# Kernel optimization log

Measured on AMD Instinct MI355X. Metric: run time of the kernel, lower is better.

The kernel has to match this reference:

```python
import jax, jax.numpy as jnp
import numpy as np

B = 48            # graph pairs
NQ, NC = 20, 16   # query / corpus node counts (corpus padded to NMAX)
NMAX = 20         # max_node_set_size
DN, DE = 16, 8    # raw node / edge feature dims
D = 32            # node_state_dim
EH = 64           # edge_hidden_sizes[-1]
EQ, EC = 80, 60   # edges per query / corpus graph
PROP = 5          # n_prop_layers
TEMP = 0.01       # sinkhorn temperature
ITERS = 20        # sinkhorn iterations
LAMBDA = 1.0
NTOT = B * (NQ + NC)
NE = B * (EQ + EC)
SRC, DST = np.triu_indices(NMAX, 1)   # nC2 = 190 node pairs
_indq = np.ones(NMAX, np.int32)
_indc = np.array([1] * NC + [0] * (NMAX - NC), np.int32)
NXOR = jnp.asarray((_indq[:, None] ^ _indc[None, :]).astype(np.float32))  # [20,20]


def _mlp2(x, w1, b1, w2, b2):
    return jnp.maximum(x @ w1 + b1, 0.0) @ w2 + b2


def _sinkhorn(log_alpha):
    la = log_alpha / TEMP
    for _ in range(ITERS):
        la = la - jax.nn.logsumexp(la, axis=2, keepdims=True)
        la = la - jax.nn.logsumexp(la, axis=1, keepdims=True)
    return jnp.exp(la)


def _edge_emb(H, adj, w1, b1, w2, b2):
    s, d = H[:, SRC], H[:, DST]            # [B,nC2,D] gathers
    e = adj[:, SRC, DST][..., None]        # [B,nC2,1]
    f = _mlp2(jnp.concatenate([s, d, e], -1), w1, b1, w2, b2)
    bk = _mlp2(jnp.concatenate([d, s, e], -1), w1, b1, w2, b2)
    return f + bk                          # bidirectional msg, [B,nC2,EH]


def _forward(node_features, edge_features, query_adj, corpus_adj,
             enc_nw, enc_nb, enc_ew, enc_eb,
             msg_w1, msg_b1, msg_w2, msg_b2,
             upd_w1, upd_b1, upd_w2, upd_b2,
             sink_w1, sink_b1, sink_w2, sink_b2,
             lrl_w1, lrl_b1, lrl_w2, lrl_b2,
             from_idx, to_idx):
    h = node_features @ enc_nw + enc_nb    # GMN encoder (linear MLPs)
    e = edge_features @ enc_ew + enc_eb
    for _ in range(PROP):                  # shared-param propagation
        msg = _mlp2(jnp.concatenate([h[from_idx], h[to_idx], e], -1),
                    msg_w1, msg_b1, msg_w2, msg_b2)
        agg = jax.ops.segment_sum(msg, to_idx, num_segments=NTOT)
        h = h + _mlp2(jnp.concatenate([agg, h], -1), upd_w1, upd_b1, upd_w2, upd_b2)
    hp = h.reshape(B, NQ + NC, D)          # split_and_stack (static sizes)
    Hq = hp[:, :NQ]
    Hc = jnp.pad(hp[:, NQ:], ((0, 0), (0, NMAX - NC), (0, 0)))
    tq = _mlp2(Hq, sink_w1, sink_b1, sink_w2, sink_b2)
    tc = _mlp2(Hc, sink_w1, sink_b1, sink_w2, sink_b2)
    cost = jnp.abs(tq[:, :, None, :] - tc[:, None, :, :]).sum(-1)  # cdist p=1
    P = _sinkhorn(-cost)                   # node transport plan [B,20,20]
    Eq = _edge_emb(Hq, query_adj, lrl_w1, lrl_b1, lrl_w2, lrl_b2)
    Ec = _edge_emb(Hc, corpus_adj, lrl_w1, lrl_b1, lrl_w2, lrl_b2)
    Pa, Pb = P[:, SRC, :], P[:, DST, :]
    straight = Pa[:, :, SRC] * Pb[:, :, DST]    # plan[src_i,src_j]*plan[dst_i,dst_j]
    cross = Pa[:, :, DST] * Pb[:, :, SRC]
    eT = straight + cross                  # use_max=False, no second sinkhorn
    aq = query_adj[:, SRC, DST].astype(jnp.int32)
    ac = corpus_adj[:, SRC, DST].astype(jnp.int32)
    pxor = (aq[:, :, None] ^ ac[:, None, :]).astype(P.dtype)
    ediff = Eq[:, :, None, :] - Ec[:, None, :, :]   # [B,nC2,nC2,EH]
    ecost = jnp.maximum(ediff, 0.0).sum(-1) + jnp.maximum(-ediff, 0.0).sum(-1)
    edge_align = (pxor * eT * ecost).sum((-1, -2))
    ndiff = Hq[:, :, None, :] - Hc[:, None, :, :]   # [B,20,20,D]
    ncost = jnp.maximum(ndiff, 0.0).sum(-1) + jnp.maximum(-ndiff, 0.0).sum(-1)
    node_align = (NXOR * P * ncost).sum((-1, -2))
    return edge_align + LAMBDA * node_align         # [B]


def setup_inputs():
    key = jax.random.key(0)
    rng = np.random.default_rng(0)
    base = (np.arange(B) * (NQ + NC))[:, None]
    fq = base + rng.integers(0, NQ, (B, EQ)); tq = base + rng.integers(0, NQ, (B, EQ))
    fc = base + NQ + rng.integers(0, NC, (B, EC)); tc = base + NQ + rng.integers(0, NC, (B, EC))
    from_idx = jnp.asarray(np.concatenate([fq, fc], 1).reshape(-1), jnp.int32)
    to_idx = jnp.asarray(np.concatenate([tq, tc], 1).reshape(-1), jnp.int32)
    qadj = rng.integers(0, 2, (B, NMAX, NMAX)).astype(np.float32)
    cadj = rng.integers(0, 2, (B, NMAX, NMAX)).astype(np.float32)
    cadj[:, NC:, :] = 0.0; cadj[:, :, NC:] = 0.0   # padded corpus nodes have no edges
    ks = iter(jax.random.split(key, 32))
    def w(shape, s=0.1):
        return jax.random.normal(next(ks), shape, jnp.float32) * s
    return {
        'node_features': w((NTOT, DN), 1.0),
        'edge_features': w((NE, DE), 1.0),
        'query_adj': jnp.asarray(qadj),
        'corpus_adj': jnp.asarray(cadj),
        'enc_nw': w((DN, D)), 'enc_nb': w((D,)),
        'enc_ew': w((DE, 16)), 'enc_eb': w((16,)),
        'msg_w1': w((2 * D + 16, EH)), 'msg_b1': w((EH,)),
        'msg_w2': w((EH, EH)), 'msg_b2': w((EH,)),
        'upd_w1': w((EH + D, EH)), 'upd_b1': w((EH,)),
        'upd_w2': w((EH, D)), 'upd_b2': w((D,)),
        'sink_w1': w((D, NMAX)), 'sink_b1': w((NMAX,)),
        'sink_w2': w((NMAX, NMAX)), 'sink_b2': w((NMAX,)),
        'lrl_w1': w((2 * D + 1, EH)), 'lrl_b1': w((EH,)),
        'lrl_w2': w((EH, EH)), 'lrl_b2': w((EH,)),
        'from_idx': from_idx, 'to_idx': to_idx,
        'graph_sizes': jnp.asarray(np.tile([NQ, NC], B), jnp.int32),
    }


def reference(node_features, edge_features, query_adj, corpus_adj,
              enc_nw, enc_nb, enc_ew, enc_eb,
              msg_w1, msg_b1, msg_w2, msg_b2,
              upd_w1, upd_b1, upd_w2, upd_b2,
              sink_w1, sink_b1, sink_w2, sink_b2,
              lrl_w1, lrl_b1, lrl_w2, lrl_b2,
              from_idx, to_idx, graph_sizes):
    return _forward(node_features, edge_features, query_adj, corpus_adj,
                    enc_nw, enc_nb, enc_ew, enc_eb,
                    msg_w1, msg_b1, msg_w2, msg_b2,
                    upd_w1, upd_b1, upd_w2, upd_b2,
                    sink_w1, sink_b1, sink_w2, sink_b2,
                    lrl_w1, lrl_b1, lrl_w2, lrl_b2,
                    from_idx, to_idx)
```

## Files before the change

### kernel.cpp

```cpp
#include <hip/hip_runtime.h>


constexpr int kB    = 48;
constexpr int kNM   = 20;
constexpr int kD    = 32;
constexpr int kNP   = 190;
constexpr int kNTOT = 1728;
constexpr int kIters = 20;
constexpr float kInvT = 100.0f;

__device__ __forceinline__ void pair_sd(int p, int& s, int& d) {
    int row = 0, rem = p;
    #pragma unroll
    for (int r = 0; r < 19; ++r) {
        int len = 19 - r;
        if (rem < len) { row = r; break; }
        rem -= len;
    }
    s = row; d = row + 1 + rem;
}

__device__ __forceinline__ float bc(float v, int k) {
    return __int_as_float(__builtin_amdgcn_readlane(__float_as_int(v), k));
}

__device__ __forceinline__ void lse20(float (&r)[20]) {
    float m01 = fmaxf(r[0], r[1]),  m23 = fmaxf(r[2], r[3]),
          m45 = fmaxf(r[4], r[5]),  m67 = fmaxf(r[6], r[7]),
          m89 = fmaxf(r[8], r[9]),  mab = fmaxf(r[10], r[11]),
          mcd = fmaxf(r[12], r[13]), mef = fmaxf(r[14], r[15]),
          mgh = fmaxf(r[16], r[17]), mij = fmaxf(r[18], r[19]);
    float n0 = fmaxf(m01, m23), n1 = fmaxf(m45, m67), n2 = fmaxf(m89, mab),
          n3 = fmaxf(mcd, mef), n4 = fmaxf(mgh, mij);
    float m = fmaxf(fmaxf(fmaxf(n0, n1), fmaxf(n2, n3)), n4);
    float e[20];
    #pragma unroll
    for (int k = 0; k < 20; ++k) e[k] = __expf(r[k] - m);
    float s01 = e[0] + e[1],  s23 = e[2] + e[3],  s45 = e[4] + e[5],
          s67 = e[6] + e[7],  s89 = e[8] + e[9],  sab = e[10] + e[11],
          scd = e[12] + e[13], sef = e[14] + e[15], sgh = e[16] + e[17],
          sij = e[18] + e[19];
    float t0 = s01 + s23, t1 = s45 + s67, t2 = s89 + sab,
          t3 = scd + sef, t4 = sgh + sij;
    float s = ((t0 + t1) + (t2 + t3)) + t4;
    float l = m + __logf(s);
    #pragma unroll
    for (int k = 0; k < 20; ++k) r[k] -= l;
}

__global__ void k_enc(const float* __restrict__ nf, const float* __restrict__ nw,
                      const float* __restrict__ nb, const float* __restrict__ ef,
                      const float* __restrict__ ew, const float* __restrict__ eb,
                      float* __restrict__ h, float* __restrict__ ee,
                      float* __restrict__ agg, float* __restrict__ out) {
    int tid = blockIdx.x * 256 + threadIdx.x;
    int stride = gridDim.x * 256;
    for (int i = tid; i < kNTOT * 32; i += stride) {
        int n = i >> 5, c = i & 31;
        float acc = nb[c];
        const float* row = nf + n * 16;
        #pragma unroll
        for (int k = 0; k < 16; ++k) acc = fmaf(row[k], nw[k * 32 + c], acc);
        h[i] = acc;
    }
    for (int i = tid; i < 6720 * 16; i += stride) {
        int n = i >> 4, c = i & 15;
        float acc = eb[c];
        const float* row = ef + n * 8;
        #pragma unroll
        for (int k = 0; k < 8; ++k) acc = fmaf(row[k], ew[k * 16 + c], acc);
        ee[i] = acc;
    }
    for (int i = tid; i < kNTOT * 64; i += stride) agg[i] = 0.f;
    if (tid < kB) out[tid] = 0.f;
}

__global__ void k_msg(const float* __restrict__ h, const float* __restrict__ ee,
                      const int* __restrict__ fidx, const int* __restrict__ tidx,
                      const float* __restrict__ w1, const float* __restrict__ b1,
                      const float* __restrict__ w2, const float* __restrict__ b2,
                      float* __restrict__ agg) {
    __shared__ float xs[4][80];
    __shared__ float hs[4][64];
    int w = threadIdx.x >> 6, lane = threadIdx.x & 63;
    int e = blockIdx.x * 4 + w;
    int from = fidx[e], to = tidx[e];
    if (lane < 32) xs[w][lane] = h[from * kD + lane];
    else           xs[w][lane] = h[to * kD + (lane - 32)];
    if (lane < 16) xs[w][64 + lane] = ee[e * 16 + lane];
    __syncthreads();
    float acc = b1[lane];
    #pragma unroll 8
    for (int k = 0; k < 80; ++k) acc += xs[w][k] * w1[k * 64 + lane];
    hs[w][lane] = fmaxf(acc, 0.f);
    __syncthreads();
    float o = b2[lane];
    #pragma unroll 8
    for (int k = 0; k < 64; ++k) o += hs[w][k] * w2[k * 64 + lane];
    atomicAdd(&agg[to * 64 + lane], o);
}

__global__ void k_upd(float* __restrict__ h, float* __restrict__ agg,
                      const float* __restrict__ w1, const float* __restrict__ b1,
                      const float* __restrict__ w2, const float* __restrict__ b2) {
    __shared__ float xs[4][96];
    __shared__ float hs[4][64];
    int w = threadIdx.x >> 6, lane = threadIdx.x & 63;
    int n = blockIdx.x * 4 + w;
    xs[w][lane] = agg[n * 64 + lane];
    agg[n * 64 + lane] = 0.f;
    if (lane < 32) xs[w][64 + lane] = h[n * kD + lane];
    __syncthreads();
    float acc = b1[lane];
    #pragma unroll 8
    for (int k = 0; k < 96; ++k) acc += xs[w][k] * w1[k * 64 + lane];
    hs[w][lane] = fmaxf(acc, 0.f);
    __syncthreads();
    if (lane < 32) {
        float o = b2[lane];
        #pragma unroll 8
        for (int k = 0; k < 64; ++k) o += hs[w][k] * w2[k * 32 + lane];
        h[n * kD + lane] += o;
    }
}

__global__ void k_sink_t(const float* __restrict__ h,
                         const float* __restrict__ w1, const float* __restrict__ b1,
                         const float* __restrict__ w2, const float* __restrict__ b2,
                         float* __restrict__ Hq, float* __restrict__ Hc,
                         float* __restrict__ tq, float* __restrict__ tc) {
    __shared__ float xs[4][32];
    __shared__ float hs[4][20];
    int w = threadIdx.x >> 6, lane = threadIdx.x & 63;
    int id = blockIdx.x * 4 + w;
    int side = id / (kB * kNM);
    int rem  = id % (kB * kNM);
    int b = rem / kNM, i = rem % kNM;
    if (lane < 32) {
        float v;
        if (side == 0) v = h[(b * 36 + i) * kD + lane];
        else           v = (i < 16) ? h[(b * 36 + 20 + i) * kD + lane] : 0.f;
        (side ? Hc : Hq)[(b * kNM + i) * kD + lane] = v;
        xs[w][lane] = v;
    }
    __syncthreads();
    if (lane < kNM) {
        float acc = b1[lane];
        #pragma unroll
        for (int k = 0; k < kD; ++k) acc += xs[w][k] * w1[k * kNM + lane];
        hs[w][lane] = fmaxf(acc, 0.f);
    }
    __syncthreads();
    if (lane < kNM) {
        float o = b2[lane];
        #pragma unroll
        for (int k = 0; k < kNM; ++k) o += hs[w][k] * w2[k * kNM + lane];
        (side ? tc : tq)[(b * kNM + i) * kNM + lane] = o;
    }
}

__global__ void k_sinkhorn(const float* __restrict__ tq, const float* __restrict__ tc,
                           const float* __restrict__ Hq,
                           float* __restrict__ P, float* __restrict__ out) {
    __shared__ float tcS[400];
    __shared__ float tr[20 * 21];
    int b = blockIdx.x, lane = threadIdx.x;
    for (int i = lane; i < 400; i += 64) tcS[i] = tc[b * 400 + i];
    int i20 = lane < 20 ? lane : 0;
    float tqr[20];
    #pragma unroll
    for (int k = 0; k < 20; ++k) tqr[k] = tq[(b * 20 + i20) * 20 + k];
    __syncthreads();
    float r[20];
    #pragma unroll
    for (int j = 0; j < 20; ++j) {
        float c = 0.f;
        #pragma unroll
        for (int k = 0; k < 20; ++k) c += fabsf(tqr[k] - tcS[j * 20 + k]);
        r[j] = -c * kInvT;
    }
    for (int it = 0; it < kIters; ++it) {
        lse20(r);
        if (lane < 20) {
            #pragma unroll
            for (int j = 0; j < 20; ++j) tr[lane * 21 + j] = r[j];
        }
        __syncthreads();
        if (lane < 20) {
            #pragma unroll
            for (int i = 0; i < 20; ++i) r[i] = tr[i * 21 + lane];
        }
        __syncthreads();
        lse20(r);
        if (lane < 20) {
            #pragma unroll
            for (int i = 0; i < 20; ++i) tr[i * 21 + lane] = r[i];
        }
        __syncthreads();
        if (lane < 20) {
            #pragma unroll
            for (int j = 0; j < 20; ++j) r[j] = tr[lane * 21 + j];
        }
        __syncthreads();
    }
    float part = 0.f;
    if (lane < 20) {
        float pv[20];
        #pragma unroll
        for (int j = 0; j < 20; ++j) pv[j] = __expf(r[j]);
        float* Pb = P + b * 400 + lane * 20;
        #pragma unroll
        for (int j = 0; j < 20; ++j) Pb[j] = pv[j];
        float pr4 = (pv[16] + pv[17]) + (pv[18] + pv[19]);
        float l1 = 0.f;
        const float* hq = Hq + (b * 20 + lane) * 32;
        #pragma unroll
        for (int k = 0; k < 32; ++k) l1 += fabsf(hq[k]);
        part = pr4 * l1;
    }
    #pragma unroll
    for (int off = 32; off; off >>= 1) part += __shfl_down(part, off, 64);
    if (lane == 0) atomicAdd(&out[b], part);
}

__global__ void k_edge_emb(const float* __restrict__ Hq, const float* __restrict__ Hc,
                           const float* __restrict__ qadj, const float* __restrict__ cadj,
                           const float* __restrict__ w1, const float* __restrict__ b1,
                           const float* __restrict__ w2, const float* __restrict__ b2,
                           float* __restrict__ Eq, float* __restrict__ Ec) {
    __shared__ float xs[4][66];
    __shared__ float hs[4][64];
    int w = threadIdx.x >> 6, lane = threadIdx.x & 63;
    int id = blockIdx.x * 4 + w;
    int side = id / (kB * kNP);
    int rem  = id % (kB * kNP);
    int b = rem / kNP, p = rem % kNP;
    int sp, dp; pair_sd(p, sp, dp);
    const float* H   = side ? Hc : Hq;
    const float* adj = side ? cadj : qadj;
    if (lane < 32) xs[w][lane] = H[(b * kNM + sp) * kD + lane];
    else           xs[w][lane] = H[(b * kNM + dp) * kD + (lane - 32)];
    if (lane == 0) xs[w][64] = adj[b * 400 + sp * 20 + dp];
    __syncthreads();
    float af = b1[lane], ab = af;
    #pragma unroll 8
    for (int k = 0; k < 64; ++k) {
        float wk = w1[k * 64 + lane];
        af += xs[w][k] * wk;
        ab += xs[w][(k + 32) & 63] * wk;
    }
    {
        float wk = w1[64 * 64 + lane];
        float ev = xs[w][64];
        af += ev * wk; ab += ev * wk;
    }
    hs[w][lane] = fmaxf(af, 0.f) + fmaxf(ab, 0.f);
    __syncthreads();
    float o = 2.f * b2[lane];
    #pragma unroll 8
    for (int k = 0; k < 64; ++k) o += hs[w][k] * w2[k * 64 + lane];
    (side ? Ec : Eq)[(b * kNP + p) * 64 + lane] = o;
}

__global__ void __launch_bounds__(256, 4)
k_final(const float* __restrict__ P, const float* __restrict__ Eq,
        const float* __restrict__ Ec, const float* __restrict__ qadj,
        const float* __restrict__ cadj, float* __restrict__ out) {
    __shared__ float Ps[400];
    __shared__ unsigned char spsh[192], dpsh[192];
    int b = blockIdx.x / 6, qt = blockIdx.x % 6;
    int t = threadIdx.x, w = t >> 6, lane = t & 63;
    if (t < 192) {
        int s = 0, d = 0;
        if (t < kNP) pair_sd(t, s, d);
        spsh[t] = (unsigned char)s;
        dpsh[t] = (unsigned char)d;
    }
    for (int i = t; i < 400; i += 256) Ps[i] = P[b * 400 + i];
    __syncthreads();

    int l31 = lane & 31;
    int q = qt * 32 + l31;
    bool qv = q < kNP;
    int sq = spsh[qv ? q : 0], dq = dpsh[qv ? q : 0];
    float acv = qv ? cadj[b * 400 + sq * 20 + dq] : 0.f;

    float ec[32];
    #pragma unroll
    for (int j = 0; j < 32; ++j) {
        int qq = qt * 32 + j;
        ec[j] = (qq < kNP) ? Ec[(b * kNP + qq) * 64 + lane] : 0.f;
    }

    float a0 = 0.f, a1 = 0.f, a2 = 0.f, a3 = 0.f;
    for (int pp = w; pp < kNP; pp += 4) {
        int sp = spsh[pp], dp = dpsh[pp];
        float aq = qadj[b * 400 + sp * 20 + dp];
        float eT = Ps[sp * 20 + sq] * Ps[dp * 20 + dq]
                 + Ps[sp * 20 + dq] * Ps[dp * 20 + sq];
        float wqv = qv ? ((aq > 0.5f) ? (1.f - acv) : acv) * eT : 0.f;
        float eqv = Eq[(b * kNP + pp) * 64 + lane];
        #pragma unroll
        for (int j = 0; j < 32; j += 4) {
            a0 = fmaf(bc(wqv, j + 0), fabsf(eqv - ec[j + 0]), a0);
            a1 = fmaf(bc(wqv, j + 1), fabsf(eqv - ec[j + 1]), a1);
            a2 = fmaf(bc(wqv, j + 2), fabsf(eqv - ec[j + 2]), a2);
            a3 = fmaf(bc(wqv, j + 3), fabsf(eqv - ec[j + 3]), a3);
        }
    }
    float partial = (a0 + a1) + (a2 + a3);
    #pragma unroll
    for (int off = 32; off; off >>= 1) partial += __shfl_down(partial, off, 64);
    if (lane == 0) atomicAdd(&out[b], partial);
}

extern "C" void kernel_launch(void* const* d_in, const int* in_sizes, int n_in,
                              void* d_out, int out_size, void* d_ws, size_t ws_size,
                              hipStream_t stream) {
    auto f = [&](int i) { return (const float*)d_in[i]; };
    const float* nf   = f(0);
    const float* ef   = f(1);
    const float* qadj = f(2);
    const float* cadj = f(3);
    const int* from_idx = (const int*)d_in[24];
    const int* to_idx   = (const int*)d_in[25];
    float* out = (float*)d_out;

    float* ws  = (float*)d_ws;
    float* h   = ws;
    float* ee  = h   + 55296;
    float* agg = ee  + 107520;
    float* Hq  = agg + 110592;
    float* Hc  = Hq  + 30720;
    float* tq  = Hc  + 30720;
    float* tc  = tq  + 19200;
    float* P   = tc  + 19200;
    float* Eq  = P   + 19200;
    float* Ec  = Eq  + 583680;

    k_enc<<<432, 256, 0, stream>>>(nf, f(4), f(5), ef, f(6), f(7), h, ee, agg, out);
    for (int it = 0; it < 5; ++it) {
        k_msg<<<1680, 256, 0, stream>>>(h, ee, from_idx, to_idx,
                                        f(8), f(9), f(10), f(11), agg);
        k_upd<<<432, 256, 0, stream>>>(h, agg, f(12), f(13), f(14), f(15));
    }
    k_sink_t<<<480, 256, 0, stream>>>(h, f(16), f(17), f(18), f(19), Hq, Hc, tq, tc);
    k_sinkhorn<<<48, 64, 0, stream>>>(tq, tc, Hq, P, out);
    k_edge_emb<<<4560, 256, 0, stream>>>(Hq, Hc, qadj, cadj,
                                         f(20), f(21), f(22), f(23), Eq, Ec);
    k_final<<<288, 256, 0, stream>>>(P, Eq, Ec, qadj, cadj, out);
}
```

Baseline: 178.0 us.

## Register-block message/update MLPs, fuse Sinkhorn into edge-embedding launch, split final reduction

The message and update MLP kernels now give each wavefront four edges or nodes. Inputs are broadcast with readlane instead of being staged in shared memory, so each weight load is reused four times and the block syncs go away. The serial Sinkhorn kernel is merged into the edge-embedding launch as 48 extra blocks, so its long dependent loop overlaps with the embedding work instead of running alone. The final kernel splits the pair loop over four times as many blocks to raise parallelism. The costs are more atomics per output in the final step, higher register pressure, and fewer blocks for the propagation kernels.

```diff
diff --git a/kernel.cpp b/kernel.cpp
--- a/kernel.cpp
+++ b/kernel.cpp
@@ -8,6 +8,8 @@
 constexpr int kNTOT = 1728;
 constexpr int kIters = 20;
 constexpr float kInvT = 100.0f;
+
+constexpr int kEmbBlocks = 4560;
 
 __device__ __forceinline__ void pair_sd(int p, int& s, int& d) {
     int row = 0, rem = p;
@@ -75,52 +77,85 @@
     if (tid < kB) out[tid] = 0.f;
 }
 
-__global__ void k_msg(const float* __restrict__ h, const float* __restrict__ ee,
-                      const int* __restrict__ fidx, const int* __restrict__ tidx,
-                      const float* __restrict__ w1, const float* __restrict__ b1,
-                      const float* __restrict__ w2, const float* __restrict__ b2,
-                      float* __restrict__ agg) {
-    __shared__ float xs[4][80];
-    __shared__ float hs[4][64];
+__global__ void __launch_bounds__(256)
+k_msg(const float* __restrict__ h, const float* __restrict__ ee,
+      const int* __restrict__ fidx, const int* __restrict__ tidx,
+      const float* __restrict__ w1, const float* __restrict__ b1,
+      const float* __restrict__ w2, const float* __restrict__ b2,
+      float* __restrict__ agg) {
     int w = threadIdx.x >> 6, lane = threadIdx.x & 63;
-    int e = blockIdx.x * 4 + w;
-    int from = fidx[e], to = tidx[e];
-    if (lane < 32) xs[w][lane] = h[from * kD + lane];
-    else           xs[w][lane] = h[to * kD + (lane - 32)];
-    if (lane < 16) xs[w][64 + lane] = ee[e * 16 + lane];
-    __syncthreads();
-    float acc = b1[lane];
-    #pragma unroll 8
-    for (int k = 0; k < 80; ++k) acc += xs[w][k] * w1[k * 64 + lane];
-    hs[w][lane] = fmaxf(acc, 0.f);
-    __syncthreads();
-    float o = b2[lane];
-    #pragma unroll 8
-    for (int k = 0; k < 64; ++k) o += hs[w][k] * w2[k * 64 + lane];
-    atomicAdd(&agg[to * 64 + lane], o);
-}
-
-__global__ void k_upd(float* __restrict__ h, float* __restrict__ agg,
-                      const float* __restrict__ w1, const float* __restrict__ b1,
-                      const float* __restrict__ w2, const float* __restrict__ b2) {
-    __shared__ float xs[4][96];
-    __shared__ float hs[4][64];
+    int e0 = (blockIdx.x * 4 + w) * 4;
+    int toj[4]; float xa[4], xb[4], acc[4], o[4];
+    #pragma unroll
+    for (int j = 0; j < 4; ++j) {
+        int e = e0 + j;
+        int fr = fidx[e]; toj[j] = tidx[e];
+        xa[j] = h[(lane < 32 ? fr : toj[j]) * kD + (lane & 31)];
+        xb[j] = ee[e * 16 + (lane & 15)];
+        acc[j] = b1[lane];
+    }
+    #pragma unroll
+    for (int k = 0; k < 64; ++k) {
+        float w1k = w1[k * 64 + lane];
+        #pragma unroll
+        for (int j = 0; j < 4; ++j) acc[j] = fmaf(bc(xa[j], k), w1k, acc[j]);
+    }
+    #pragma unroll
+    for (int k = 0; k < 16; ++k) {
+        float w1k = w1[(64 + k) * 64 + lane];
+        #pragma unroll
+        for (int j = 0; j < 4; ++j) acc[j] = fmaf(bc(xb[j], k), w1k, acc[j]);
+    }
+    #pragma unroll
+    for (int j = 0; j < 4; ++j) { acc[j] = fmaxf(acc[j], 0.f); o[j] = b2[lane]; }
+    #pragma unroll
+    for (int k = 0; k < 64; ++k) {
+        float w2k = w2[k * 64 + lane];
+        #pragma unroll
+        for (int j = 0; j < 4; ++j) o[j] = fmaf(bc(acc[j], k), w2k, o[j]);
+    }
+    #pragma unroll
+    for (int j = 0; j < 4; ++j) atomicAdd(&agg[toj[j] * 64 + lane], o[j]);
+}
+
+__global__ void __launch_bounds__(256)
+k_upd(float* __restrict__ h, float* __restrict__ agg,
+      const float* __restrict__ w1, const float* __restrict__ b1,
+      const float* __restrict__ w2, const float* __restrict__ b2) {
     int w = threadIdx.x >> 6, lane = threadIdx.x & 63;
-    int n = blockIdx.x * 4 + w;
-    xs[w][lane] = agg[n * 64 + lane];
-    agg[n * 64 + lane] = 0.f;
-    if (lane < 32) xs[w][64 + lane] = h[n * kD + lane];
-    __syncthreads();
-    float acc = b1[lane];
-    #pragma unroll 8
-    for (int k = 0; k < 96; ++k) acc += xs[w][k] * w1[k * 64 + lane];
-    hs[w][lane] = fmaxf(acc, 0.f);
-    __syncthreads();
+    int n0 = (blockIdx.x * 4 + w) * 4;
+    float xa[4], xb[4], acc[4], o[4];
+    #pragma unroll
+    for (int j = 0; j < 4; ++j) {
+        int n = n0 + j;
+        xa[j] = agg[n * 64 + lane];
+        agg[n * 64 + lane] = 0.f;
+        xb[j] = h[n * kD + (lane & 31)];
+        acc[j] = b1[lane];
+    }
+    #pragma unroll
+    for (int k = 0; k < 64; ++k) {
+        float w1k = w1[k * 64 + lane];
+        #pragma unroll
+        for (int j = 0; j < 4; ++j) acc[j] = fmaf(bc(xa[j], k), w1k, acc[j]);
+    }
+    #pragma unroll
+    for (int k = 0; k < 32; ++k) {
+        float w1k = w1[(64 + k) * 64 + lane];
+        #pragma unroll
+        for (int j = 0; j < 4; ++j) acc[j] = fmaf(bc(xb[j], k), w1k, acc[j]);
+    }
+    #pragma unroll
+    for (int j = 0; j < 4; ++j) { acc[j] = fmaxf(acc[j], 0.f); o[j] = b2[lane & 31]; }
+    #pragma unroll
+    for (int k = 0; k < 64; ++k) {
+        float w2k = w2[k * 32 + (lane & 31)];
+        #pragma unroll
+        for (int j = 0; j < 4; ++j) o[j] = fmaf(bc(acc[j], k), w2k, o[j]);
+    }
     if (lane < 32) {
-        float o = b2[lane];
-        #pragma unroll 8
-        for (int k = 0; k < 64; ++k) o += hs[w][k] * w2[k * 32 + lane];
-        h[n * kD + lane] += o;
+        #pragma unroll
+        for (int j = 0; j < 4; ++j) h[(n0 + j) * kD + lane] += o[j];
     }
 }
 
@@ -159,78 +194,80 @@
     }
 }
 
-__global__ void k_sinkhorn(const float* __restrict__ tq, const float* __restrict__ tc,
-                           const float* __restrict__ Hq,
-                           float* __restrict__ P, float* __restrict__ out) {
-    __shared__ float tcS[400];
-    __shared__ float tr[20 * 21];
-    int b = blockIdx.x, lane = threadIdx.x;
-    for (int i = lane; i < 400; i += 64) tcS[i] = tc[b * 400 + i];
-    int i20 = lane < 20 ? lane : 0;
-    float tqr[20];
-    #pragma unroll
-    for (int k = 0; k < 20; ++k) tqr[k] = tq[(b * 20 + i20) * 20 + k];
-    __syncthreads();
-    float r[20];
-    #pragma unroll
-    for (int j = 0; j < 20; ++j) {
-        float c = 0.f;
-        #pragma unroll
-        for (int k = 0; k < 20; ++k) c += fabsf(tqr[k] - tcS[j * 20 + k]);
-        r[j] = -c * kInvT;
-    }
-    for (int it = 0; it < kIters; ++it) {
-        lse20(r);
-        if (lane < 20) {
-            #pragma unroll
-            for (int j = 0; j < 20; ++j) tr[lane * 21 + j] = r[j];
-        }
-        __syncthreads();
-        if (lane < 20) {
-            #pragma unroll
-            for (int i = 0; i < 20; ++i) r[i] = tr[i * 21 + lane];
-        }
-        __syncthreads();
-        lse20(r);
-        if (lane < 20) {
-            #pragma unroll
-            for (int i = 0; i < 20; ++i) tr[i * 21 + lane] = r[i];
-        }
-        __syncthreads();
-        if (lane < 20) {
-            #pragma unroll
-            for (int j = 0; j < 20; ++j) r[j] = tr[lane * 21 + j];
-        }
-        __syncthreads();
-    }
-    float part = 0.f;
-    if (lane < 20) {
-        float pv[20];
-        #pragma unroll
-        for (int j = 0; j < 20; ++j) pv[j] = __expf(r[j]);
-        float* Pb = P + b * 400 + lane * 20;
-        #pragma unroll
-        for (int j = 0; j < 20; ++j) Pb[j] = pv[j];
-        float pr4 = (pv[16] + pv[17]) + (pv[18] + pv[19]);
-        float l1 = 0.f;
-        const float* hq = Hq + (b * 20 + lane) * 32;
-        #pragma unroll
-        for (int k = 0; k < 32; ++k) l1 += fabsf(hq[k]);
-        part = pr4 * l1;
-    }
-    #pragma unroll
-    for (int off = 32; off; off >>= 1) part += __shfl_down(part, off, 64);
-    if (lane == 0) atomicAdd(&out[b], part);
-}
-
-__global__ void k_edge_emb(const float* __restrict__ Hq, const float* __restrict__ Hc,
+__global__ void k_emb_sink(const float* __restrict__ Hq, const float* __restrict__ Hc,
                            const float* __restrict__ qadj, const float* __restrict__ cadj,
                            const float* __restrict__ w1, const float* __restrict__ b1,
                            const float* __restrict__ w2, const float* __restrict__ b2,
-                           float* __restrict__ Eq, float* __restrict__ Ec) {
+                           const float* __restrict__ tq, const float* __restrict__ tc,
+                           float* __restrict__ Eq, float* __restrict__ Ec,
+                           float* __restrict__ P, float* __restrict__ out) {
     __shared__ float xs[4][66];
     __shared__ float hs[4][64];
-    int w = threadIdx.x >> 6, lane = threadIdx.x & 63;
+    __shared__ float tcS[400];
+    __shared__ float tr[20 * 21];
+    int t = threadIdx.x, w = t >> 6, lane = t & 63;
+
+    if (blockIdx.x >= kEmbBlocks) {
+        int b = blockIdx.x - kEmbBlocks;
+        for (int i = t; i < 400; i += 256) tcS[i] = tc[b * 400 + i];
+        int i20 = t < 20 ? t : 0;
+        float tqr[20];
+        #pragma unroll
+        for (int k = 0; k < 20; ++k) tqr[k] = tq[(b * 20 + i20) * 20 + k];
+        __syncthreads();
+        float r[20];
+        #pragma unroll
+        for (int j = 0; j < 20; ++j) {
+            float c = 0.f;
+            #pragma unroll
+            for (int k = 0; k < 20; ++k) c += fabsf(tqr[k] - tcS[j * 20 + k]);
+            r[j] = -c * kInvT;
+        }
+        for (int it = 0; it < kIters; ++it) {
+            lse20(r);
+            if (t < 20) {
+                #pragma unroll
+                for (int j = 0; j < 20; ++j) tr[t * 21 + j] = r[j];
+            }
+            __syncthreads();
+            if (t < 20) {
+                #pragma unroll
+                for (int i = 0; i < 20; ++i) r[i] = tr[i * 21 + t];
+            }
+            __syncthreads();
+            lse20(r);
+            if (t < 20) {
+                #pragma unroll
+                for (int i = 0; i < 20; ++i) tr[i * 21 + t] = r[i];
+            }
+            __syncthreads();
+            if (t < 20) {
+                #pragma unroll
+                for (int j = 0; j < 20; ++j) r[j] = tr[t * 21 + j];
+            }
+            __syncthreads();
+        }
+        float part = 0.f;
+        if (t < 20) {
+            float pv[20];
+            #pragma unroll
+            for (int j = 0; j < 20; ++j) pv[j] = __expf(r[j]);
+            float* Pb = P + b * 400 + t * 20;
+            #pragma unroll
+            for (int j = 0; j < 20; ++j) Pb[j] = pv[j];
+            float pr4 = (pv[16] + pv[17]) + (pv[18] + pv[19]);
+            float l1 = 0.f;
+            const float* hq = Hq + (b * 20 + t) * 32;
+            #pragma unroll
+            for (int k = 0; k < 32; ++k) l1 += fabsf(hq[k]);
+            part = pr4 * l1;
+        }
+        #pragma unroll
+        for (int off = 32; off; off >>= 1) part += __shfl_down(part, off, 64);
+        if (t == 0) atomicAdd(&out[b], part);
+        return;
+    }
+
     int id = blockIdx.x * 4 + w;
     int side = id / (kB * kNP);
     int rem  = id % (kB * kNP);
@@ -268,7 +305,9 @@
         const float* __restrict__ cadj, float* __restrict__ out) {
     __shared__ float Ps[400];
     __shared__ unsigned char spsh[192], dpsh[192];
-    int b = blockIdx.x / 6, qt = blockIdx.x % 6;
+    int b = blockIdx.x / 24;
+    int r = blockIdx.x % 24;
+    int qt = r >> 2, pc = r & 3;
     int t = threadIdx.x, w = t >> 6, lane = t & 63;
     if (t < 192) {
         int s = 0, d = 0;
@@ -293,7 +332,7 @@
     }
 
     float a0 = 0.f, a1 = 0.f, a2 = 0.f, a3 = 0.f;
-    for (int pp = w; pp < kNP; pp += 4) {
+    for (int pp = pc * 4 + w; pp < kNP; pp += 16) {
         int sp = spsh[pp], dp = dpsh[pp];
         float aq = qadj[b * 400 + sp * 20 + dp];
         float eT = Ps[sp * 20 + sq] * Ps[dp * 20 + dq]
@@ -340,13 +379,13 @@
 
     k_enc<<<432, 256, 0, stream>>>(nf, f(4), f(5), ef, f(6), f(7), h, ee, agg, out);
     for (int it = 0; it < 5; ++it) {
-        k_msg<<<1680, 256, 0, stream>>>(h, ee, from_idx, to_idx,
-                                        f(8), f(9), f(10), f(11), agg);
-        k_upd<<<432, 256, 0, stream>>>(h, agg, f(12), f(13), f(14), f(15));
+        k_msg<<<420, 256, 0, stream>>>(h, ee, from_idx, to_idx,
+                                       f(8), f(9), f(10), f(11), agg);
+        k_upd<<<108, 256, 0, stream>>>(h, agg, f(12), f(13), f(14), f(15));
     }
     k_sink_t<<<480, 256, 0, stream>>>(h, f(16), f(17), f(18), f(19), Hq, Hc, tq, tc);
-    k_sinkhorn<<<48, 64, 0, stream>>>(tq, tc, Hq, P, out);
-    k_edge_emb<<<4560, 256, 0, stream>>>(Hq, Hc, qadj, cadj,
-                                         f(20), f(21), f(22), f(23), Eq, Ec);
-    k_final<<<288, 256, 0, stream>>>(P, Eq, Ec, qadj, cadj, out);
-}
+    k_emb_sink<<<kEmbBlocks + kB, 256, 0, stream>>>(Hq, Hc, qadj, cadj,
+                                                    f(20), f(21), f(22), f(23),
+                                                    tq, tc, Eq, Ec, P, out);
+    k_final<<<1152, 256, 0, stream>>>(P, Eq, Ec, qadj, cadj, out);
+}
```

After: 179.2 us. Within noise of the previous version (+0.7%).
